# Performance work log

Hardware: AMD Instinct MI355X
Metric: run time of the kernel (lower is better)

The kernel has to match this reference:

```python
import jax, jax.numpy as jnp
import numpy as np

B, C, H, W_SP = 64, 16, 8, 8
IN_DIM, MIDDLE, NUM_CLASSES = 2048, 8192, 2048
K_ITERS, TAU, NUM_GROUPS = 1024, 0.5, 8
SPLIT = NUM_GROUPS * 7 * 7  # 392
BN_EPS = 1e-5


def setup_inputs() -> dict:
    key = jax.random.key(0)
    ks = jax.random.split(key, 20)
    f = jax.random.normal(ks[0], (B, C, H, W_SP), jnp.float32)

    def lin(kw, kb, fan_out, fan_in):
        lim = 1.0 / np.sqrt(fan_in)
        W = jax.random.uniform(kw, (fan_out, fan_in), jnp.float32, -lim, lim)
        b = jax.random.uniform(kb, (fan_out,), jnp.float32, -lim, lim)
        return W, b

    def bn_stats(km, kv, n):
        rm = 0.1 * jax.random.normal(km, (n,), jnp.float32)
        rv = jax.random.uniform(kv, (n,), jnp.float32, 0.5, 1.5)
        return rm, rv

    W1, b1 = lin(ks[1], ks[2], MIDDLE, IN_DIM)
    g1 = 1.0 + 0.1 * jax.random.normal(ks[3], (MIDDLE,), jnp.float32)
    beta1 = 0.1 * jax.random.normal(ks[4], (MIDDLE,), jnp.float32)
    rm1, rv1 = bn_stats(ks[5], ks[6], MIDDLE)

    W2, b2 = lin(ks[7], ks[8], MIDDLE, MIDDLE)
    g2 = 1.0 + 0.1 * jax.random.normal(ks[9], (MIDDLE,), jnp.float32)
    beta2 = 0.1 * jax.random.normal(ks[10], (MIDDLE,), jnp.float32)
    rm2, rv2 = bn_stats(ks[11], ks[12], MIDDLE)

    W3, b3 = lin(ks[13], ks[14], NUM_CLASSES, MIDDLE)
    rm3, rv3 = bn_stats(ks[15], ks[16], NUM_CLASSES)  # final BN, affine=False

    return {"f": f, "W1": W1, "b1": b1, "g1": g1, "beta1": beta1, "rm1": rm1, "rv1": rv1,
            "W2": W2, "b2": b2, "g2": g2, "beta2": beta2, "rm2": rm2, "rv2": rv2,
            "W3": W3, "b3": b3, "rm3": rm3, "rv3": rv3}


def _bn(x, rm, rv, g=None, b=None):
    y = (x - rm) / jnp.sqrt(rv + BN_EPS)
    if g is not None:
        y = y * g + b
    return y


def reference(f, W1, b1, g1, beta1, rm1, rv1, W2, b2, g2, beta2, rm2, rv2, W3, b3, rm3, rv3):
    # FFT over spatial axes; the original code overwrites abs/angle with the raw
    # complex array twice, then the torch dtype cast drops the imaginary part.
    f_fft = jnp.fft.fft2(f, axes=(2, 3))
    flat = jnp.real(f_fft).reshape(B, -1).astype(f.dtype)  # [64, 1024]
    x = jnp.concatenate([flat, flat], axis=1)              # [64, 2048]

    # MLP in eval mode (Dropout = identity, BatchNorm uses running stats)
    h = jax.nn.relu(_bn(x @ W1.T + b1, rm1, rv1, g1, beta1))
    h = jax.nn.relu(_bn(h @ W2.T + b2, rm2, rv2, g2, beta2))
    mask = _bn(h @ W3.T + b3, rm3, rv3)                    # [64, 2048]

    # Iterated gumbel-softmax with running max, k=1024 iterations
    keys = jax.random.split(jax.random.key(42), K_ITERS)
    tiny = jnp.finfo(mask.dtype).tiny

    def step(carry, k):
        m, z = carry
        u = jax.random.uniform(k, m.shape, m.dtype, minval=tiny, maxval=1.0)
        gum = -jnp.log(-jnp.log(u))
        m = jax.nn.softmax((m + gum) / TAU, axis=1)
        z = jnp.maximum(m, z)
        return (m, z), None

    (_, z), _ = jax.lax.scan(step, (mask, jnp.zeros_like(mask)), keys)
    return z[:, :SPLIT], z[:, SPLIT:]
```

## Files before the change

kernel.cpp:

```cpp
#include <hip/hip_runtime.h>
#include <hip/hip_bf16.h>
#include <stdint.h>

__device__ __forceinline__ uint32_t rotl32(uint32_t v, int s) {
    return (v << s) | (v >> (32 - s));
}

__device__ __forceinline__ void tf2x32(uint32_t k0, uint32_t k1,
                                       uint32_t x0, uint32_t x1,
                                       uint32_t& o0, uint32_t& o1) {
    uint32_t ks2 = k0 ^ k1 ^ 0x1BD11BDAu;
    x0 += k0; x1 += k1;
#define TFR(R0,R1,R2,R3) \
    x0 += x1; x1 = rotl32(x1, R0); x1 ^= x0; \
    x0 += x1; x1 = rotl32(x1, R1); x1 ^= x0; \
    x0 += x1; x1 = rotl32(x1, R2); x1 ^= x0; \
    x0 += x1; x1 = rotl32(x1, R3); x1 ^= x0;
    TFR(13,15,26,6)   x0 += k1;  x1 += ks2 + 1u;
    TFR(17,29,16,24)  x0 += ks2; x1 += k0  + 2u;
    TFR(13,15,26,6)   x0 += k0;  x1 += k1  + 3u;
    TFR(17,29,16,24)  x0 += k1;  x1 += ks2 + 4u;
    TFR(13,15,26,6)   x0 += ks2; x1 += k0  + 5u;
#undef TFR
    o0 = x0; o1 = x1;
}

__device__ __forceinline__ uint32_t pbits32(uint32_t k0, uint32_t k1, uint32_t ctr) {
    uint32_t o0, o1;
    tf2x32(k0, k1, 0u, ctr, o0, o1);
    return o0 ^ o1;
}

#define NROW 64
#define NCOL 2048
#define NFLAT 131072
#define SPLIT 392
#define C2 2.8853900817779268f

__device__ __forceinline__ float gumbel_from_bits(uint32_t bits) {
    const float TINY = 1.17549435e-38f;
    float f = (float)(bits >> 9) * 1.1920928955078125e-7f;
    float u = fmaxf(TINY, f + TINY);
    return -logf(-logf(u));
}

template<int CTRL, int RM>
__device__ __forceinline__ float dpp_add(float s) {
    int x = __builtin_amdgcn_update_dpp(0, __builtin_bit_cast(int, s),
                                        CTRL, RM, 0xf, true);
    return s + __builtin_bit_cast(float, x);
}

__device__ __forceinline__ float wave_sum64(float v) {
    v = dpp_add<0x111, 0xf>(v);
    v = dpp_add<0x112, 0xf>(v);
    v = dpp_add<0x114, 0xf>(v);
    v = dpp_add<0x118, 0xf>(v);
    v = dpp_add<0x142, 0xa>(v);
    v = dpp_add<0x143, 0xc>(v);
    return __builtin_bit_cast(float,
        __builtin_amdgcn_readlane(__builtin_bit_cast(int, v), 63));
}

__global__ __launch_bounds__(256) void keygenF(uint32_t* __restrict__ kb) {
    int n = blockIdx.x * 256 + threadIdx.x;
    uint32_t o0, o1;
    tf2x32(0u, 42u, 0u, (uint32_t)n, o0, o1);
    kb[2 * n] = o0;
    kb[2 * n + 1] = o1;
}

__device__ __constant__ float c_ctab[8] = {
    1.0f, 0.70710678118654752f, 0.0f, -0.70710678118654752f,
   -1.0f, -0.70710678118654752f, 0.0f, 0.70710678118654752f
};

__global__ __launch_bounds__(256) void fft_x(const float* __restrict__ f,
                                             float* __restrict__ x) {
    int gid = blockIdx.x * 256 + threadIdx.x;
    int b = gid >> 10, i = gid & 1023;
    int c = i >> 6, h = (i >> 3) & 7, w = i & 7;
    const float* fb = f + ((b << 4) + c) * 64;
    float s = 0.0f;
#pragma unroll
    for (int hp = 0; hp < 8; ++hp) {
#pragma unroll
        for (int wp = 0; wp < 8; ++wp)
            s += fb[hp * 8 + wp] * c_ctab[(h * hp + w * wp) & 7];
    }
    x[b * NCOL + i] = s;
    x[b * NCOL + 1024 + i] = s;
}

__global__ __launch_bounds__(256) void prep(
    const float* __restrict__ b1, const float* __restrict__ g1,
    const float* __restrict__ be1, const float* __restrict__ rm1, const float* __restrict__ rv1,
    const float* __restrict__ b2, const float* __restrict__ g2,
    const float* __restrict__ be2, const float* __restrict__ rm2, const float* __restrict__ rv2,
    float* __restrict__ s1, float* __restrict__ o1,
    float* __restrict__ s2, float* __restrict__ o2) {
    int i = blockIdx.x * 256 + threadIdx.x;
    const float eps = 1e-5f;
    float inv = 1.0f / sqrtf(rv1[i] + eps);
    float s = g1[i] * inv;
    s1[i] = s; o1[i] = (b1[i] - rm1[i]) * s + be1[i];
    inv = 1.0f / sqrtf(rv2[i] + eps);
    s = g2[i] * inv;
    s2[i] = s; o2[i] = (b2[i] - rm2[i]) * s + be2[i];
}

template<bool AFF>
__global__ __launch_bounds__(256)
void gemm_ks(const float* __restrict__ A,
             const float* __restrict__ sA, const float* __restrict__ oA,
             const float* __restrict__ B, float* __restrict__ Cpart,
             int K, int Kc, int N) {
    __shared__ __align__(16) float As[64 * 36];
    __shared__ __align__(16) float Bs[128 * 36];
    const int t = threadIdx.x;
    const int n0 = blockIdx.x * 128;
    const int k0 = blockIdx.y * Kc;
    const int tm = t >> 4, tn = t & 15;

    float acc[4][8];
#pragma unroll
    for (int i = 0; i < 4; ++i)
#pragma unroll
        for (int j = 0; j < 8; ++j) acc[i][j] = 0.0f;

    for (int kt = k0; kt < k0 + Kc; kt += 32) {
#pragma unroll
        for (int h = 0; h < 2; ++h) {
            int idx = h * 1024 + t * 4;
            int am = idx >> 5, ak = idx & 31;
            float4 v = *(const float4*)(A + (size_t)am * K + kt + ak);
            if (AFF) {
                float4 s = *(const float4*)(sA + kt + ak);
                float4 o = *(const float4*)(oA + kt + ak);
                v.x = fmaxf(v.x * s.x + o.x, 0.0f);
                v.y = fmaxf(v.y * s.y + o.y, 0.0f);
                v.z = fmaxf(v.z * s.z + o.z, 0.0f);
                v.w = fmaxf(v.w * s.w + o.w, 0.0f);
            }
            *(float4*)&As[am * 36 + (ak ^ (((am >> 2) & 7) << 2))] = v;
        }
#pragma unroll
        for (int h = 0; h < 4; ++h) {
            int idx = h * 1024 + t * 4;
            int bn = idx >> 5, bk = idx & 31;
            float4 v = *(const float4*)(B + (size_t)(n0 + bn) * K + kt + bk);
            *(float4*)&Bs[bn * 36 + (bk ^ (((bn >> 3) & 7) << 2))] = v;
        }
        __syncthreads();
#pragma unroll
        for (int kbk = 0; kbk < 8; ++kbk) {
            float4 a[4], b[8];
            int acol = (kbk * 4) ^ ((tm & 7) << 2);
#pragma unroll
            for (int i = 0; i < 4; ++i)
                a[i] = *(const float4*)&As[(tm * 4 + i) * 36 + acol];
            int bcol = (kbk * 4) ^ ((tn & 7) << 2);
#pragma unroll
            for (int j = 0; j < 8; ++j)
                b[j] = *(const float4*)&Bs[(tn * 8 + j) * 36 + bcol];
#pragma unroll
            for (int i = 0; i < 4; ++i)
#pragma unroll
                for (int j = 0; j < 8; ++j) {
                    acc[i][j] = fmaf(a[i].x, b[j].x, acc[i][j]);
                    acc[i][j] = fmaf(a[i].y, b[j].y, acc[i][j]);
                    acc[i][j] = fmaf(a[i].z, b[j].z, acc[i][j]);
                    acc[i][j] = fmaf(a[i].w, b[j].w, acc[i][j]);
                }
        }
        __syncthreads();
    }
#pragma unroll
    for (int i = 0; i < 4; ++i) {
        size_t co = (size_t)blockIdx.y * ((size_t)64 * N)
                  + (size_t)((tm << 2) + i) * N + n0 + (tn << 3);
        float4 v0 = {acc[i][0], acc[i][1], acc[i][2], acc[i][3]};
        float4 v1 = {acc[i][4], acc[i][5], acc[i][6], acc[i][7]};
        *(float4*)(Cpart + co) = v0;
        *(float4*)(Cpart + co + 4) = v1;
    }
}

__global__ __launch_bounds__(256) void combineP(const float* __restrict__ parts,
                                                float* __restrict__ dst,
                                                int P, int total) {
    int gid = blockIdx.x * 256 + threadIdx.x;
    if (gid >= total) return;
    float s = 0.0f;
    for (int p = 0; p < P; ++p) s += parts[(size_t)p * total + gid];
    dst[gid] = s;
}

__global__ __launch_bounds__(256) void combine3(const float* __restrict__ parts,
                                                const float* __restrict__ b3,
                                                const float* __restrict__ rm3,
                                                const float* __restrict__ rv3,
                                                float* __restrict__ mstate, int P) {
    int gid = blockIdx.x * 256 + threadIdx.x;
    int c = gid & 2047;
    float v = 0.0f;
    for (int p = 0; p < P; ++p) v += parts[(size_t)p * NFLAT + gid];
    mstate[gid] = (v + b3[c] - rm3[c]) / sqrtf(rv3[c] + 1e-5f);
}

__global__ __launch_bounds__(1024)
void hash_chunk(const uint32_t* __restrict__ kb, float* __restrict__ gbuf,
                int t0, int Tc) {
    size_t total = (size_t)Tc * NFLAT;
    for (size_t idx = (size_t)blockIdx.x * 1024 + threadIdx.x; idx < total;
         idx += (size_t)gridDim.x * 1024) {
        int tt = (int)(idx >> 17);
        int j  = (int)(idx & (NFLAT - 1));
        int tg = t0 + tt;
        uint32_t k0 = kb[2 * tg], k1 = kb[2 * tg + 1];
        gbuf[idx] = gumbel_from_bits(pbits32(k0, k1, (uint32_t)j)) * C2;
    }
}

__global__ __launch_bounds__(1024)
void scan_fused(float* __restrict__ mstate, float* __restrict__ zstate,
                const float* __restrict__ gscan,
                float* __restrict__ hdst, int ht0, int hcnt,
                const uint32_t* __restrict__ kb,
                int t0, int Tc, int last, float* __restrict__ out) {
    const int tid = threadIdx.x;

    if (blockIdx.x >= 64) {
        if (hcnt <= 0) return;
        int hb = blockIdx.x - 64;
        size_t total = (size_t)hcnt * NFLAT;
        for (size_t idx = (size_t)hb * 1024 + tid; idx < total;
             idx += (size_t)192 * 1024) {
            int tt = (int)(idx >> 17);
            int j  = (int)(idx & (NFLAT - 1));
            int tg = ht0 + tt;
            uint32_t k0 = kb[2 * tg], k1 = kb[2 * tg + 1];
            hdst[idx] = gumbel_from_bits(pbits32(k0, k1, (uint32_t)j)) * C2;
        }
        return;
    }

    __shared__ __align__(16) float red[2][16];
    const int r = blockIdx.x;
    const int c0 = tid, c1 = tid + 1024;
    const int base = r * NCOL;
    float m0 = mstate[base + c0], m1 = mstate[base + c1];
    float z0, z1;
    if (t0 == 0) { z0 = 0.0f; z1 = 0.0f; }
    else         { z0 = zstate[base + c0]; z1 = zstate[base + c1]; }
    const int lane = tid & 63, wid = tid >> 6;

    float g0 = gscan[base + c0];
    float g1 = gscan[base + c1];
    for (int tt = 0; tt < Tc; ++tt) {
        float cg0 = g0, cg1 = g1;
        if (tt + 1 < Tc) {
            size_t ao = (size_t)(tt + 1) * NFLAT + base;
            g0 = gscan[ao + c0];
            g1 = gscan[ao + c1];
        }
        float p0 = exp2f(fmaf(m0, C2, cg0));
        float p1 = exp2f(fmaf(m1, C2, cg1));
        float ws = wave_sum64(p0 + p1);
        if (lane == 0) red[tt & 1][wid] = ws;
        __syncthreads();
        float S;
        {
            const float4* r4 = (const float4*)&red[tt & 1][0];
            float4 v0 = r4[0], v1 = r4[1], v2 = r4[2], v3 = r4[3];
            S = ((v0.x + v0.y) + (v0.z + v0.w)) + ((v1.x + v1.y) + (v1.z + v1.w))
              + ((v2.x + v2.y) + (v2.z + v2.w)) + ((v3.x + v3.y) + (v3.z + v3.w));
        }
        float rs = __builtin_amdgcn_rcpf(S);
        m0 = p0 * rs; m1 = p1 * rs;
        z0 = fmaxf(z0, m0); z1 = fmaxf(z1, m1);
    }
    mstate[base + c0] = m0; mstate[base + c1] = m1;
    zstate[base + c0] = z0; zstate[base + c1] = z1;
    if (last) {
        if (c0 < SPLIT) out[r * SPLIT + c0] = z0;
        else out[64 * SPLIT + r * (NCOL - SPLIT) + (c0 - SPLIT)] = z0;
        out[64 * SPLIT + r * (NCOL - SPLIT) + (c1 - SPLIT)] = z1;
    }
}

__global__ __launch_bounds__(1024)
void scan_inline(const float* __restrict__ mstate, const uint32_t* __restrict__ kb,
                 float* __restrict__ out) {
    const int r = blockIdx.x;
    const int tid = threadIdx.x;
    const int c0 = tid, c1 = tid + 1024;
    const int base = r * NCOL;
    float m0 = mstate[base + c0], m1 = mstate[base + c1];
    float z0 = 0.0f, z1 = 0.0f;
    __shared__ __align__(16) float red[2][16];
    const int lane = tid & 63, wid = tid >> 6;

    for (int t = 0; t < 1024; ++t) {
        uint32_t k0 = kb[2 * t], k1 = kb[2 * t + 1];
        float g0 = gumbel_from_bits(pbits32(k0, k1, (uint32_t)(base + c0)));
        float g1 = gumbel_from_bits(pbits32(k0, k1, (uint32_t)(base + c1)));
        float p0 = exp2f((m0 + g0) * C2);
        float p1 = exp2f((m1 + g1) * C2);
        float ws = wave_sum64(p0 + p1);
        if (lane == 0) red[t & 1][wid] = ws;
        __syncthreads();
        float S;
        {
            const float4* r4 = (const float4*)&red[t & 1][0];
            float4 v0 = r4[0], v1 = r4[1], v2 = r4[2], v3 = r4[3];
            S = ((v0.x + v0.y) + (v0.z + v0.w)) + ((v1.x + v1.y) + (v1.z + v1.w))
              + ((v2.x + v2.y) + (v2.z + v2.w)) + ((v3.x + v3.y) + (v3.z + v3.w));
        }
        float rs = __builtin_amdgcn_rcpf(S);
        m0 = p0 * rs; m1 = p1 * rs;
        z0 = fmaxf(z0, m0); z1 = fmaxf(z1, m1);
    }
    if (c0 < SPLIT) out[r * SPLIT + c0] = z0;
    else out[64 * SPLIT + r * (NCOL - SPLIT) + (c0 - SPLIT)] = z0;
    out[64 * SPLIT + r * (NCOL - SPLIT) + (c1 - SPLIT)] = z1;
}

extern "C" void kernel_launch(void* const* d_in, const int* in_sizes, int n_in,
                              void* d_out, int out_size, void* d_ws, size_t ws_size,
                              hipStream_t stream) {
    const float* f   = (const float*)d_in[0];
    const float* W1  = (const float*)d_in[1];
    const float* b1  = (const float*)d_in[2];
    const float* g1  = (const float*)d_in[3];
    const float* be1 = (const float*)d_in[4];
    const float* rm1 = (const float*)d_in[5];
    const float* rv1 = (const float*)d_in[6];
    const float* W2  = (const float*)d_in[7];
    const float* b2  = (const float*)d_in[8];
    const float* g2  = (const float*)d_in[9];
    const float* be2 = (const float*)d_in[10];
    const float* rm2 = (const float*)d_in[11];
    const float* rv2 = (const float*)d_in[12];
    const float* W3  = (const float*)d_in[13];
    const float* b3  = (const float*)d_in[14];
    const float* rm3 = (const float*)d_in[15];
    const float* rv3 = (const float*)d_in[16];
    float* out = (float*)d_out;

    float* ws = (float*)d_ws;
    size_t off = 0;
    auto alloc = [&](size_t n) { float* p = ws + off; off += n; return p; };

    uint32_t* keybuf = (uint32_t*)alloc(2048);
    float* s1 = alloc(8192); float* o1 = alloc(8192);
    float* s2 = alloc(8192); float* o2 = alloc(8192);
    float* x      = alloc(64 * 2048);
    float* h1     = alloc((size_t)64 * 8192);
    float* h2     = alloc((size_t)64 * 8192);
    float* mstate = alloc(NFLAT);
    float* zstate = alloc(NFLAT);
    size_t fixed = off;
    float* pbuf = ws + fixed;
    size_t region = (ws_size / 4 > fixed) ? (ws_size / 4 - fixed) : 0;

    const size_t HN = (size_t)64 * 8192;
    const size_t GALL = (size_t)1024 * NFLAT;

    keygenF<<<dim3(4), 256, 0, stream>>>(keybuf);
    prep<<<dim3(32), 256, 0, stream>>>(b1, g1, be1, rm1, rv1,
                                       b2, g2, be2, rm2, rv2,
                                       s1, o1, s2, o2);
    fft_x<<<dim3(256), 256, 0, stream>>>(f, x);

    if (region >= GALL + 32 * HN) {
        float* gbufAll = pbuf;
        float* parts   = pbuf + GALL;

        gemm_ks<false><<<dim3(64, 16), 256, 0, stream>>>(
            x, nullptr, nullptr, W1, parts, 2048, 128, 8192);
        combineP<<<dim3(2048), 256, 0, stream>>>(parts, h1, 16, (int)HN);
        gemm_ks<true><<<dim3(64, 32), 256, 0, stream>>>(
            h1, s1, o1, W2, parts, 8192, 256, 8192);
        combineP<<<dim3(2048), 256, 0, stream>>>(parts, h2, 32, (int)HN);
        gemm_ks<true><<<dim3(16, 32), 256, 0, stream>>>(
            h2, s2, o2, W3, parts, 8192, 256, 2048);
        combine3<<<dim3(512), 256, 0, stream>>>(parts, b3, rm3, rv3, mstate, 32);

        hash_chunk<<<dim3(256), 1024, 0, stream>>>(keybuf, gbufAll, 0, 256);
        for (int ch = 0; ch < 8; ++ch) {
            int hstart = 256 + ch * 128;
            int hcnt = (hstart < 1024) ? 128 : 0;
            scan_fused<<<dim3(256), 1024, 0, stream>>>(
                mstate, zstate, gbufAll + (size_t)ch * 128 * NFLAT,
                gbufAll + (size_t)hstart * NFLAT, hstart, hcnt, keybuf,
                ch * 128, 128, (ch == 7) ? 1 : 0, out);
        }
    } else {
        int KS1 = (region >= 8 * HN) ? 8 : (region >= 4 * HN) ? 4 :
                  (region >= 2 * HN) ? 2 : 1;
        int KS2 = (region >= 16 * HN) ? 16 : (region >= 8 * HN) ? 8 :
                  (region >= 4 * HN) ? 4 : (region >= 2 * HN) ? 2 : 1;
        int KS3 = (region >= 16 * (size_t)NFLAT) ? 16 :
                  (region >= 8 * (size_t)NFLAT) ? 8 :
                  (region >= 4 * (size_t)NFLAT) ? 4 :
                  (region >= 2 * (size_t)NFLAT) ? 2 : 1;
        int Tc = 0;
        const int cands[5] = {128, 64, 32, 16, 8};
        for (int ci = 0; ci < 5; ++ci)
            if (2 * (size_t)cands[ci] * NFLAT <= region) { Tc = cands[ci]; break; }

        gemm_ks<false><<<dim3(64, KS1), 256, 0, stream>>>(
            x, nullptr, nullptr, W1, (KS1 > 1) ? pbuf : h1, 2048, 2048 / KS1, 8192);
        if (KS1 > 1) combineP<<<dim3(2048), 256, 0, stream>>>(pbuf, h1, KS1, (int)HN);

        gemm_ks<true><<<dim3(64, KS2), 256, 0, stream>>>(
            h1, s1, o1, W2, (KS2 > 1) ? pbuf : h2, 8192, 8192 / KS2, 8192);
        if (KS2 > 1) combineP<<<dim3(2048), 256, 0, stream>>>(pbuf, h2, KS2, (int)HN);

        if (KS3 > 1) {
            gemm_ks<true><<<dim3(16, KS3), 256, 0, stream>>>(
                h2, s2, o2, W3, pbuf, 8192, 8192 / KS3, 2048);
            combine3<<<dim3(512), 256, 0, stream>>>(pbuf, b3, rm3, rv3, mstate, KS3);
        } else {
            gemm_ks<true><<<dim3(16, 1), 256, 0, stream>>>(
                h2, s2, o2, W3, h1, 8192, 8192, 2048);
            combine3<<<dim3(512), 256, 0, stream>>>(h1, b3, rm3, rv3, mstate, 1);
        }

        if (Tc > 0) {
            float* gbuf0 = pbuf;
            float* gbuf1 = pbuf + (size_t)Tc * NFLAT;
            int NC = 1024 / Tc;
            hash_chunk<<<dim3(256), 1024, 0, stream>>>(keybuf, gbuf0, 0, Tc);
            for (int ch = 0; ch < NC; ++ch) {
                float* ga = (ch & 1) ? gbuf1 : gbuf0;
                float* gb = (ch & 1) ? gbuf0 : gbuf1;
                int last = (ch == NC - 1) ? 1 : 0;
                scan_fused<<<dim3(256), 1024, 0, stream>>>(
                    mstate, zstate, ga, gb, (ch + 1) * Tc, last ? 0 : Tc,
                    keybuf, ch * Tc, Tc, last, out);
            }
        } else {
            scan_inline<<<dim3(64), 1024, 0, stream>>>(mstate, keybuf, out);
        }
    }
}
```

Before: 962.3 us.

## Transpose GEMM smem tiles, halve split-K, deepen scan prefetch, shrink hash prologue

The GEMM now stores A and B tiles k-major in padded shared arrays, so each k-step reads one float4 of A and two of B for an outer product, replacing the XOR-swizzled row-major layout. Split-K is halved for all three GEMMs (fewer partials to combine, fewer blocks), and the fused scan prefetches gumbel values four steps ahead instead of one. The initial hash pass covers only 128 steps, with the chunk loop hashing the following chunk. The transposed scalar smem stores may bank-conflict, and halving split-K lowers the parallelism available to the GEMMs.

```diff
diff --git a/kernel.cpp b/kernel.cpp
--- a/kernel.cpp
+++ b/kernel.cpp
@@ -115,8 +115,8 @@
              const float* __restrict__ sA, const float* __restrict__ oA,
              const float* __restrict__ B, float* __restrict__ Cpart,
              int K, int Kc, int N) {
-    __shared__ __align__(16) float As[64 * 36];
-    __shared__ __align__(16) float Bs[128 * 36];
+    __shared__ float As[32][68];
+    __shared__ float Bs[32][132];
     const int t = threadIdx.x;
     const int n0 = blockIdx.x * 128;
     const int k0 = blockIdx.y * Kc;
@@ -133,7 +133,8 @@
         for (int h = 0; h < 2; ++h) {
             int idx = h * 1024 + t * 4;
             int am = idx >> 5, ak = idx & 31;
-            float4 v = *(const float4*)(A + (size_t)am * K + kt + ak);
+            size_t go = (size_t)am * K + kt + ak;
+            float4 v = *(const float4*)(A + go);
             if (AFF) {
                 float4 s = *(const float4*)(sA + kt + ak);
                 float4 o = *(const float4*)(oA + kt + ak);
@@ -142,36 +143,30 @@
                 v.z = fmaxf(v.z * s.z + o.z, 0.0f);
                 v.w = fmaxf(v.w * s.w + o.w, 0.0f);
             }
-            *(float4*)&As[am * 36 + (ak ^ (((am >> 2) & 7) << 2))] = v;
+            As[ak + 0][am] = v.x; As[ak + 1][am] = v.y;
+            As[ak + 2][am] = v.z; As[ak + 3][am] = v.w;
         }
 #pragma unroll
         for (int h = 0; h < 4; ++h) {
             int idx = h * 1024 + t * 4;
             int bn = idx >> 5, bk = idx & 31;
             float4 v = *(const float4*)(B + (size_t)(n0 + bn) * K + kt + bk);
-            *(float4*)&Bs[bn * 36 + (bk ^ (((bn >> 3) & 7) << 2))] = v;
+            Bs[bk + 0][bn] = v.x; Bs[bk + 1][bn] = v.y;
+            Bs[bk + 2][bn] = v.z; Bs[bk + 3][bn] = v.w;
         }
         __syncthreads();
-#pragma unroll
-        for (int kbk = 0; kbk < 8; ++kbk) {
-            float4 a[4], b[8];
-            int acol = (kbk * 4) ^ ((tm & 7) << 2);
+#pragma unroll 8
+        for (int kk = 0; kk < 32; ++kk) {
+            float4 av = *(const float4*)&As[kk][tm << 2];
+            float4 b0 = *(const float4*)&Bs[kk][tn << 3];
+            float4 b1 = *(const float4*)&Bs[kk][(tn << 3) + 4];
+            float a4[4] = {av.x, av.y, av.z, av.w};
+            float b8[8] = {b0.x, b0.y, b0.z, b0.w, b1.x, b1.y, b1.z, b1.w};
 #pragma unroll
             for (int i = 0; i < 4; ++i)
-                a[i] = *(const float4*)&As[(tm * 4 + i) * 36 + acol];
-            int bcol = (kbk * 4) ^ ((tn & 7) << 2);
-#pragma unroll
-            for (int j = 0; j < 8; ++j)
-                b[j] = *(const float4*)&Bs[(tn * 8 + j) * 36 + bcol];
-#pragma unroll
-            for (int i = 0; i < 4; ++i)
-#pragma unroll
-                for (int j = 0; j < 8; ++j) {
-                    acc[i][j] = fmaf(a[i].x, b[j].x, acc[i][j]);
-                    acc[i][j] = fmaf(a[i].y, b[j].y, acc[i][j]);
-                    acc[i][j] = fmaf(a[i].z, b[j].z, acc[i][j]);
-                    acc[i][j] = fmaf(a[i].w, b[j].w, acc[i][j]);
-                }
+#pragma unroll
+                for (int j = 0; j < 8; ++j)
+                    acc[i][j] = fmaf(a4[i], b8[j], acc[i][j]);
         }
         __syncthreads();
     }
@@ -255,30 +250,40 @@
     else         { z0 = zstate[base + c0]; z1 = zstate[base + c1]; }
     const int lane = tid & 63, wid = tid >> 6;
 
-    float g0 = gscan[base + c0];
-    float g1 = gscan[base + c1];
-    for (int tt = 0; tt < Tc; ++tt) {
-        float cg0 = g0, cg1 = g1;
-        if (tt + 1 < Tc) {
-            size_t ao = (size_t)(tt + 1) * NFLAT + base;
-            g0 = gscan[ao + c0];
-            g1 = gscan[ao + c1];
-        }
-        float p0 = exp2f(fmaf(m0, C2, cg0));
-        float p1 = exp2f(fmaf(m1, C2, cg1));
-        float ws = wave_sum64(p0 + p1);
-        if (lane == 0) red[tt & 1][wid] = ws;
-        __syncthreads();
-        float S;
-        {
-            const float4* r4 = (const float4*)&red[tt & 1][0];
-            float4 v0 = r4[0], v1 = r4[1], v2 = r4[2], v3 = r4[3];
-            S = ((v0.x + v0.y) + (v0.z + v0.w)) + ((v1.x + v1.y) + (v1.z + v1.w))
-              + ((v2.x + v2.y) + (v2.z + v2.w)) + ((v3.x + v3.y) + (v3.z + v3.w));
-        }
-        float rs = __builtin_amdgcn_rcpf(S);
-        m0 = p0 * rs; m1 = p1 * rs;
-        z0 = fmaxf(z0, m0); z1 = fmaxf(z1, m1);
+    float g0f[4], g1f[4];
+#pragma unroll
+    for (int d = 0; d < 4; ++d) {
+        size_t ao = (size_t)d * NFLAT + base;
+        g0f[d] = gscan[ao + c0];
+        g1f[d] = gscan[ao + c1];
+    }
+
+    for (int tb = 0; tb < Tc; tb += 4) {
+#pragma unroll
+        for (int ph = 0; ph < 4; ++ph) {
+            int tt = tb + ph;
+            float cg0 = g0f[ph], cg1 = g1f[ph];
+            if (tt + 4 < Tc) {
+                size_t ao = (size_t)(tt + 4) * NFLAT + base;
+                g0f[ph] = gscan[ao + c0];
+                g1f[ph] = gscan[ao + c1];
+            }
+            float p0 = exp2f(fmaf(m0, C2, cg0));
+            float p1 = exp2f(fmaf(m1, C2, cg1));
+            float ws = wave_sum64(p0 + p1);
+            if (lane == 0) red[tt & 1][wid] = ws;
+            __syncthreads();
+            float S;
+            {
+                const float4* r4 = (const float4*)&red[tt & 1][0];
+                float4 v0 = r4[0], v1 = r4[1], v2 = r4[2], v3 = r4[3];
+                S = ((v0.x + v0.y) + (v0.z + v0.w)) + ((v1.x + v1.y) + (v1.z + v1.w))
+                  + ((v2.x + v2.y) + (v2.z + v2.w)) + ((v3.x + v3.y) + (v3.z + v3.w));
+            }
+            float rs = __builtin_amdgcn_rcpf(S);
+            m0 = p0 * rs; m1 = p1 * rs;
+            z0 = fmaxf(z0, m0); z1 = fmaxf(z1, m1);
+        }
     }
     mstate[base + c0] = m0; mstate[base + c1] = m1;
     zstate[base + c0] = z0; zstate[base + c1] = z1;
@@ -373,23 +378,23 @@
                                        s1, o1, s2, o2);
     fft_x<<<dim3(256), 256, 0, stream>>>(f, x);
 
-    if (region >= GALL + 32 * HN) {
+    if (region >= GALL + 16 * HN) {
         float* gbufAll = pbuf;
         float* parts   = pbuf + GALL;
 
-        gemm_ks<false><<<dim3(64, 16), 256, 0, stream>>>(
-            x, nullptr, nullptr, W1, parts, 2048, 128, 8192);
-        combineP<<<dim3(2048), 256, 0, stream>>>(parts, h1, 16, (int)HN);
-        gemm_ks<true><<<dim3(64, 32), 256, 0, stream>>>(
-            h1, s1, o1, W2, parts, 8192, 256, 8192);
-        combineP<<<dim3(2048), 256, 0, stream>>>(parts, h2, 32, (int)HN);
-        gemm_ks<true><<<dim3(16, 32), 256, 0, stream>>>(
-            h2, s2, o2, W3, parts, 8192, 256, 2048);
-        combine3<<<dim3(512), 256, 0, stream>>>(parts, b3, rm3, rv3, mstate, 32);
-
-        hash_chunk<<<dim3(256), 1024, 0, stream>>>(keybuf, gbufAll, 0, 256);
+        gemm_ks<false><<<dim3(64, 8), 256, 0, stream>>>(
+            x, nullptr, nullptr, W1, parts, 2048, 256, 8192);
+        combineP<<<dim3(2048), 256, 0, stream>>>(parts, h1, 8, (int)HN);
+        gemm_ks<true><<<dim3(64, 16), 256, 0, stream>>>(
+            h1, s1, o1, W2, parts, 8192, 512, 8192);
+        combineP<<<dim3(2048), 256, 0, stream>>>(parts, h2, 16, (int)HN);
+        gemm_ks<true><<<dim3(16, 16), 256, 0, stream>>>(
+            h2, s2, o2, W3, parts, 8192, 512, 2048);
+        combine3<<<dim3(512), 256, 0, stream>>>(parts, b3, rm3, rv3, mstate, 16);
+
+        hash_chunk<<<dim3(256), 1024, 0, stream>>>(keybuf, gbufAll, 0, 128);
         for (int ch = 0; ch < 8; ++ch) {
-            int hstart = 256 + ch * 128;
+            int hstart = (ch + 1) * 128;
             int hcnt = (hstart < 1024) ? 128 : 0;
             scan_fused<<<dim3(256), 1024, 0, stream>>>(
                 mstate, zstate, gbufAll + (size_t)ch * 128 * NFLAT,
```

New measurement: 1.056 ms. 1.1x slower.
